# Performance work log

Hardware: AMD Instinct MI355X
Metric: run time of the kernel (lower is better)

Reference implementation:

```python
import jax, jax.numpy as jnp
import numpy as np

MAX_WEIGHT = 10.0  # config.max_weight
EPS = 1e-8

BATCH = 2048
VOCAB = 256
SEQ_LEN = 64
NUM_DENDRITES = SEQ_LEN * VOCAB  # 16384


def setup_inputs() -> dict:
    key = jax.random.key(0)
    k1, k2 = jax.random.split(key)
    # binary dendrite activations in {0,1}, stored as float32 as in the torch module
    binary = jax.random.randint(k1, (BATCH, NUM_DENDRITES), 0, 2).astype(jnp.float32)
    # raw_weights ~ Uniform(-1, 1) per nn.init.uniform_
    raw_weights = jax.random.uniform(k2, (VOCAB, NUM_DENDRITES), dtype=jnp.float32,
                                     minval=-1.0, maxval=1.0)
    return {"binary": binary, "raw_weights": raw_weights}


def reference(binary, raw_weights):
    # bounded positive weights: max_weight * sigmoid(raw)
    w = MAX_WEIGHT * jax.nn.sigmoid(raw_weights)            # (vocab, D)
    log_w = jnp.log(jnp.clip(w, EPS))                       # (vocab, D)
    # masked log-sum: where binary==0 the torch code uses log(1)=0, then multiplies
    # by binary anyway, so it is exactly binary @ log_w.T
    log_sum = jnp.einsum('bd,vd->bv', binary, log_w)        # (batch, vocab)
    n_active = jnp.clip(jnp.sum(binary, axis=-1, keepdims=True), 1.0)  # (batch, 1)
    logits = jnp.exp(log_sum / n_active)                    # geometric mean of fired weights
    return logits
```

## Files before the change

kernel.cpp:

```cpp
#include <hip/hip_runtime.h>

#define BATCH 2048
#define VOCAB 256
#define KDIM 16384
#define WPR (KDIM / 32)
#define BM 64
#define BK 64
#define S_SPLIT 16
#define KCHUNK (KDIM / S_SPLIT)
#define NT (KCHUNK / BK)
#define CW (KCHUNK / 32)
#define WSTRIDE 34
#define LN10 2.302585092994046f

typedef __attribute__((ext_vector_type(8))) short short8;
typedef __attribute__((ext_vector_type(4))) float f32x4;
typedef __attribute__((ext_vector_type(2))) unsigned short u16x2;

#define FENCE asm volatile("" ::: "memory")
#define BAR __builtin_amdgcn_s_barrier()
#define VMW8 asm volatile("s_waitcnt vmcnt(8)" ::: "memory")
#define VMW0 asm volatile("s_waitcnt vmcnt(0)" ::: "memory")

__device__ __forceinline__ unsigned short f2bf_rne(float f) {
  unsigned int u = __float_as_uint(f);
  u += 0x7fffu + ((u >> 16) & 1u);
  return (unsigned short)(u >> 16);
}

__device__ __forceinline__ void async16(void* lds, const void* g) {
  __builtin_amdgcn_global_load_lds(
      (const __attribute__((address_space(1))) unsigned int*)g,
      (__attribute__((address_space(3))) unsigned int*)lds, 16, 0, 0);
}

__device__ __forceinline__ unsigned int pkmul(unsigned int a, unsigned int b) {
  union { unsigned int u; u16x2 h; } x, y, r;
  x.u = a; y.u = b;
  r.h = x.h * y.h;
  return r.u;
}

__global__ __launch_bounds__(256) void k_logw(const float* __restrict__ raw,
                                              unsigned short* __restrict__ logw) {
  int i = blockIdx.x * 256 + threadIdx.x;
  float4 x = ((const float4*)raw)[i];
  ushort4 r;
  r.x = f2bf_rne(LN10 - log1pf(expf(-x.x)));
  r.y = f2bf_rne(LN10 - log1pf(expf(-x.y)));
  r.z = f2bf_rne(LN10 - log1pf(expf(-x.z)));
  r.w = f2bf_rne(LN10 - log1pf(expf(-x.w)));
  ((ushort4*)logw)[i] = r;
}

__global__ __launch_bounds__(256) void k_pack(const float* __restrict__ binary,
                                              unsigned int* __restrict__ bits,
                                              float* __restrict__ nact4) {
  const int r = blockIdx.x;
  const int t = threadIdx.x;
  const int lane = t & 63;
  const float4* src = (const float4*)(binary + (size_t)r * KDIM);
  unsigned int* wrow = bits + (size_t)r * WPR;
  float cnt = 0.f;
#pragma unroll
  for (int i = 0; i < 16; ++i) {
    float4 f = src[i * 256 + t];
    unsigned int nib = ((__float_as_uint(f.x) >> 29) & 1u) |
                       ((__float_as_uint(f.y) >> 28) & 2u) |
                       ((__float_as_uint(f.z) >> 27) & 4u) |
                       ((__float_as_uint(f.w) >> 26) & 8u);
    unsigned int v = nib, p;
    p = __shfl_xor(v, 1, 64); v = (lane & 1) ? (p | (v << 4)) : (v | (p << 4));
    p = __shfl_xor(v, 2, 64); v = (lane & 2) ? (p | (v << 8)) : (v | (p << 8));
    p = __shfl_xor(v, 4, 64); v = (lane & 4) ? (p | (v << 16)) : (v | (p << 16));
    if ((t & 7) == 0) wrow[i * 32 + (t >> 3)] = v;
    cnt += (float)__popc(v);
  }
  cnt *= 0.125f;
  cnt += __shfl_xor(cnt, 1, 64);
  cnt += __shfl_xor(cnt, 2, 64);
  cnt += __shfl_xor(cnt, 4, 64);
  cnt += __shfl_xor(cnt, 8, 64);
  cnt += __shfl_xor(cnt, 16, 64);
  cnt += __shfl_xor(cnt, 32, 64);
  if (lane == 0) nact4[r * 4 + (t >> 6)] = cnt;
}

template <int PART>
__global__ __launch_bounds__(256) void k_gemm(
    const unsigned int* __restrict__ bits, const unsigned short* __restrict__ logw,
    float* __restrict__ outp) {
  extern __shared__ char smem[];
  char* const B0 = smem;
  char* const B1 = smem + 32768;
  unsigned int* const Wb = (unsigned int*)(smem + 65536);

  const int tid = threadIdx.x;
  const int wv = tid >> 6;
  const int lane = tid & 63;
  const int l15 = lane & 15;
  const int lhi = lane >> 4;
  const int sh8 = lhi * 8;
  const int sx = blockIdx.x;
  const int m0 = blockIdx.y * BM;
  const int k0 = sx * KCHUNK;

  {
    const unsigned int* gsrc =
        bits + (size_t)(m0 + (tid >> 2)) * WPR + sx * CW + (tid & 3) * 8;
    uint4 w0 = *(const uint4*)gsrc;
    uint4 w1 = *(const uint4*)(gsrc + 4);
    unsigned int* ld = Wb + (tid >> 2) * WSTRIDE + (tid & 3) * 8;
    ld[0] = w0.x; ld[1] = w0.y; ld[2] = w0.z; ld[3] = w0.w;
    ld[4] = w1.x; ld[5] = w1.y; ld[6] = w1.z; ld[7] = w1.w;
  }
  __syncthreads();

  const unsigned short* bsrc =
      logw + (size_t)(wv * 64 + (lane >> 3)) * KDIM + k0 +
      (((lane & 7) ^ (lane >> 3)) << 3);
  const int rsw = (l15 & 7) << 4;

  f32x4 acc[4][4];
#pragma unroll
  for (int m = 0; m < 4; ++m)
#pragma unroll
    for (int n = 0; n < 4; ++n) acc[m][n] = f32x4{0.f, 0.f, 0.f, 0.f};

  auto BSTAGE = [&](int t, char* B) {
#pragma unroll
    for (int i = 0; i < 8; ++i)
      async16(B + (wv * 64 + i * 8) * 128, bsrc + (size_t)i * 8 * KDIM + t * BK);
  };
  auto COMPUTE = [&](const char* B, int t) {
    uint2 aw[4];
#pragma unroll
    for (int m = 0; m < 4; ++m)
      aw[m] = *(const uint2*)(Wb + (m * 16 + l15) * WSTRIDE + 2 * t);
#pragma unroll
    for (int ks = 0; ks < 2; ++ks) {
      const int koff = ((ks * 64) | (lhi * 16)) ^ rsw;
      short8 bf[4];
#pragma unroll
      for (int n = 0; n < 4; ++n)
        bf[n] = *(const short8*)(B + (wv * 64 + n * 16 + l15) * 128 + koff);
#pragma unroll
      for (int m = 0; m < 4; ++m) {
        const unsigned int w = ks ? aw[m].y : aw[m].x;
        const unsigned int rep = ((w >> sh8) & 0xffu) * 0x01010101u;
        union { unsigned int u[4]; short8 s; } ex;
        ex.u[0] = pkmul(rep & 0x00020001u, 0x1FC03F80u);
        ex.u[1] = pkmul(rep & 0x00080004u, 0x07F00FE0u);
        ex.u[2] = pkmul(rep & 0x00200010u, 0x01FC03F8u);
        ex.u[3] = pkmul(rep & 0x00800040u, 0x007F00FEu);
#pragma unroll
        for (int n = 0; n < 4; ++n)
          acc[m][n] = __builtin_amdgcn_mfma_f32_16x16x32_bf16(bf[n], ex.s,
                                                              acc[m][n], 0, 0, 0);
      }
    }
  };

  BSTAGE(0, B0);
  FENCE;
#pragma unroll 1
  for (int t = 0; t < NT; t += 2) {
    BSTAGE(t + 1, B1);
    FENCE; VMW8; BAR; FENCE;
    COMPUTE(B0, t);
    FENCE; BAR; FENCE;
    if (t + 2 < NT) {
      BSTAGE(t + 2, B0);
      FENCE; VMW8;
    } else {
      VMW0;
    }
    BAR; FENCE;
    COMPUTE(B1, t + 1);
    FENCE; BAR; FENCE;
  }

  if (PART) {
#pragma unroll
    for (int m = 0; m < 4; ++m) {
      float* dst = outp + ((size_t)sx * BATCH + m0 + m * 16 + l15) * VOCAB +
                   wv * 64 + lhi * 4;
#pragma unroll
      for (int n = 0; n < 4; ++n)
        *(float4*)(dst + n * 16) =
            (float4){acc[m][n][0], acc[m][n][1], acc[m][n][2], acc[m][n][3]};
    }
  } else {
#pragma unroll
    for (int m = 0; m < 4; ++m)
#pragma unroll
      for (int n = 0; n < 4; ++n)
#pragma unroll
        for (int i = 0; i < 4; ++i)
          atomicAdd(&outp[(size_t)(m0 + m * 16 + l15) * VOCAB + wv * 64 +
                          n * 16 + lhi * 4 + i],
                    acc[m][n][i]);
  }
}

__global__ __launch_bounds__(256) void k_reduce(const float* __restrict__ part,
                                                const float* __restrict__ nact4,
                                                float* __restrict__ out) {
  int b = blockIdx.x;
  int v = threadIdx.x;
  float sum = 0.f;
#pragma unroll
  for (int i = 0; i < S_SPLIT; ++i)
    sum += part[((size_t)i * BATCH + b) * VOCAB + v];
  float n = nact4[b * 4] + nact4[b * 4 + 1] + nact4[b * 4 + 2] + nact4[b * 4 + 3];
  out[(size_t)b * VOCAB + v] = expf(sum / fmaxf(n, 1.f));
}

__global__ __launch_bounds__(256) void k_out(float* __restrict__ io,
                                             const float* __restrict__ nact4) {
  int b = blockIdx.x;
  int v = threadIdx.x;
  float n = nact4[b * 4] + nact4[b * 4 + 1] + nact4[b * 4 + 2] + nact4[b * 4 + 3];
  n = fmaxf(n, 1.0f);
  size_t idx = (size_t)b * VOCAB + v;
  io[idx] = expf(io[idx] / n);
}

extern "C" void kernel_launch(void* const* d_in, const int* in_sizes, int n_in,
                              void* d_out, int out_size, void* d_ws, size_t ws_size,
                              hipStream_t stream) {
  const float* binary = (const float*)d_in[0];
  const float* raw = (const float*)d_in[1];
  float* out = (float*)d_out;
  char* ws = (char*)d_ws;

  const size_t LOGW_B = (size_t)VOCAB * KDIM * 2;
  const size_t BITS_B = (size_t)BATCH * WPR * 4;
  const size_t NACT_B = (size_t)BATCH * 4 * 4;
  const size_t PART_B = (size_t)S_SPLIT * BATCH * VOCAB * 4;
  unsigned short* logw = (unsigned short*)ws;
  unsigned int* bits = (unsigned int*)(ws + LOGW_B);
  float* nact4 = (float*)(ws + LOGW_B + BITS_B);
  float* part = (float*)(ws + LOGW_B + BITS_B + NACT_B);

  k_logw<<<(VOCAB * KDIM / 4) / 256, 256, 0, stream>>>(raw, logw);
  k_pack<<<BATCH, 256, 0, stream>>>(binary, bits, nact4);

  dim3 g(S_SPLIT, BATCH / BM);
  const size_t LDS_B = 65536 + 64 * WSTRIDE * 4;
  if (ws_size >= LOGW_B + BITS_B + NACT_B + PART_B) {
    k_gemm<1><<<g, 256, LDS_B, stream>>>(bits, logw, part);
    k_reduce<<<BATCH, VOCAB, 0, stream>>>(part, nact4, out);
  } else {
    hipMemsetAsync(out, 0, (size_t)BATCH * VOCAB * sizeof(float), stream);
    k_gemm<0><<<g, 256, LDS_B, stream>>>(bits, logw, out);
    k_out<<<BATCH, VOCAB, 0, stream>>>(out, nact4);
  }
}
```

Baseline: 241.9 us.

## Drop LDS staging in GEMM; load MFMA operands directly from global memory

The GEMM kernel no longer stages logw tiles and packed activation bits through double-buffered LDS with async loads and barriers. Each lane now loads its bf16 B fragments and bit words straight from global memory into registers inside a fully unrolled loop. The K split doubles to 32, and launch bounds ask for 3 blocks per SIMD. This aims to remove LDS traffic, barrier stalls and the LDS occupancy limit, at the cost of less coalesced global loads, heavier reliance on L2/L1, and twice as much partial-sum output for the reduce kernel.

```diff
diff --git a/kernel.cpp b/kernel.cpp
--- a/kernel.cpp
+++ b/kernel.cpp
@@ -5,33 +5,20 @@
 #define KDIM 16384
 #define WPR (KDIM / 32)
 #define BM 64
-#define BK 64
-#define S_SPLIT 16
+#define S_SPLIT 32
 #define KCHUNK (KDIM / S_SPLIT)
-#define NT (KCHUNK / BK)
+#define NT (KCHUNK / 64)
 #define CW (KCHUNK / 32)
-#define WSTRIDE 34
 #define LN10 2.302585092994046f
 
 typedef __attribute__((ext_vector_type(8))) short short8;
 typedef __attribute__((ext_vector_type(4))) float f32x4;
 typedef __attribute__((ext_vector_type(2))) unsigned short u16x2;
-
-#define FENCE asm volatile("" ::: "memory")
-#define BAR __builtin_amdgcn_s_barrier()
-#define VMW8 asm volatile("s_waitcnt vmcnt(8)" ::: "memory")
-#define VMW0 asm volatile("s_waitcnt vmcnt(0)" ::: "memory")
 
 __device__ __forceinline__ unsigned short f2bf_rne(float f) {
   unsigned int u = __float_as_uint(f);
   u += 0x7fffu + ((u >> 16) & 1u);
   return (unsigned short)(u >> 16);
-}
-
-__device__ __forceinline__ void async16(void* lds, const void* g) {
-  __builtin_amdgcn_global_load_lds(
-      (const __attribute__((address_space(1))) unsigned int*)g,
-      (__attribute__((address_space(3))) unsigned int*)lds, 16, 0, 0);
 }
 
 __device__ __forceinline__ unsigned int pkmul(unsigned int a, unsigned int b) {
@@ -87,14 +74,9 @@
 }
 
 template <int PART>
-__global__ __launch_bounds__(256) void k_gemm(
+__global__ __launch_bounds__(256, 3) void k_gemm(
     const unsigned int* __restrict__ bits, const unsigned short* __restrict__ logw,
     float* __restrict__ outp) {
-  extern __shared__ char smem[];
-  char* const B0 = smem;
-  char* const B1 = smem + 32768;
-  unsigned int* const Wb = (unsigned int*)(smem + 65536);
-
   const int tid = threadIdx.x;
   const int wv = tid >> 6;
   const int lane = tid & 63;
@@ -103,23 +85,15 @@
   const int sh8 = lhi * 8;
   const int sx = blockIdx.x;
   const int m0 = blockIdx.y * BM;
-  const int k0 = sx * KCHUNK;
-
-  {
-    const unsigned int* gsrc =
-        bits + (size_t)(m0 + (tid >> 2)) * WPR + sx * CW + (tid & 3) * 8;
-    uint4 w0 = *(const uint4*)gsrc;
-    uint4 w1 = *(const uint4*)(gsrc + 4);
-    unsigned int* ld = Wb + (tid >> 2) * WSTRIDE + (tid & 3) * 8;
-    ld[0] = w0.x; ld[1] = w0.y; ld[2] = w0.z; ld[3] = w0.w;
-    ld[4] = w1.x; ld[5] = w1.y; ld[6] = w1.z; ld[7] = w1.w;
-  }
-  __syncthreads();
-
-  const unsigned short* bsrc =
-      logw + (size_t)(wv * 64 + (lane >> 3)) * KDIM + k0 +
-      (((lane & 7) ^ (lane >> 3)) << 3);
-  const int rsw = (l15 & 7) << 4;
+
+  const unsigned short* bb0 = logw + (size_t)(wv * 64 + l15) * KDIM + sx * KCHUNK + lhi * 8;
+  const unsigned short* bb1 = bb0 + (size_t)16 * KDIM;
+  const unsigned short* bb2 = bb0 + (size_t)32 * KDIM;
+  const unsigned short* bb3 = bb0 + (size_t)48 * KDIM;
+  const unsigned int* wp0 = bits + (size_t)(m0 + l15) * WPR + sx * CW;
+  const unsigned int* wp1 = wp0 + 16 * WPR;
+  const unsigned int* wp2 = wp0 + 32 * WPR;
+  const unsigned int* wp3 = wp0 + 48 * WPR;
 
   f32x4 acc[4][4];
 #pragma unroll
@@ -127,57 +101,43 @@
 #pragma unroll
     for (int n = 0; n < 4; ++n) acc[m][n] = f32x4{0.f, 0.f, 0.f, 0.f};
 
-  auto BSTAGE = [&](int t, char* B) {
-#pragma unroll
-    for (int i = 0; i < 8; ++i)
-      async16(B + (wv * 64 + i * 8) * 128, bsrc + (size_t)i * 8 * KDIM + t * BK);
-  };
-  auto COMPUTE = [&](const char* B, int t) {
-    uint2 aw[4];
-#pragma unroll
-    for (int m = 0; m < 4; ++m)
-      aw[m] = *(const uint2*)(Wb + (m * 16 + l15) * WSTRIDE + 2 * t);
-#pragma unroll
-    for (int ks = 0; ks < 2; ++ks) {
-      const int koff = ((ks * 64) | (lhi * 16)) ^ rsw;
-      short8 bf[4];
-#pragma unroll
-      for (int n = 0; n < 4; ++n)
-        bf[n] = *(const short8*)(B + (wv * 64 + n * 16 + l15) * 128 + koff);
-#pragma unroll
-      for (int m = 0; m < 4; ++m) {
-        const unsigned int w = ks ? aw[m].y : aw[m].x;
-        const unsigned int rep = ((w >> sh8) & 0xffu) * 0x01010101u;
-        union { unsigned int u[4]; short8 s; } ex;
-        ex.u[0] = pkmul(rep & 0x00020001u, 0x1FC03F80u);
-        ex.u[1] = pkmul(rep & 0x00080004u, 0x07F00FE0u);
-        ex.u[2] = pkmul(rep & 0x00200010u, 0x01FC03F8u);
-        ex.u[3] = pkmul(rep & 0x00800040u, 0x007F00FEu);
-#pragma unroll
-        for (int n = 0; n < 4; ++n)
-          acc[m][n] = __builtin_amdgcn_mfma_f32_16x16x32_bf16(bf[n], ex.s,
-                                                              acc[m][n], 0, 0, 0);
+#pragma unroll
+  for (int j = 0; j < NT / 2; ++j) {
+    uint4 w0 = *(const uint4*)(wp0 + 4 * j);
+    uint4 w1 = *(const uint4*)(wp1 + 4 * j);
+    uint4 w2 = *(const uint4*)(wp2 + 4 * j);
+    uint4 w3 = *(const uint4*)(wp3 + 4 * j);
+#pragma unroll
+    for (int h = 0; h < 2; ++h) {
+      const int off = (2 * j + h) * 64;
+      short8 bf[4][2];
+#pragma unroll
+      for (int ks = 0; ks < 2; ++ks) {
+        bf[0][ks] = *(const short8*)(bb0 + off + ks * 32);
+        bf[1][ks] = *(const short8*)(bb1 + off + ks * 32);
+        bf[2][ks] = *(const short8*)(bb2 + off + ks * 32);
+        bf[3][ks] = *(const short8*)(bb3 + off + ks * 32);
+      }
+#pragma unroll
+      for (int ks = 0; ks < 2; ++ks) {
+#pragma unroll
+        for (int m = 0; m < 4; ++m) {
+          const uint4 wm = (m == 0) ? w0 : (m == 1) ? w1 : (m == 2) ? w2 : w3;
+          const unsigned int word =
+              h ? (ks ? wm.w : wm.z) : (ks ? wm.y : wm.x);
+          const unsigned int rep = ((word >> sh8) & 0xffu) * 0x01010101u;
+          union { unsigned int u[4]; short8 s; } ex;
+          ex.u[0] = pkmul(rep & 0x00020001u, 0x1FC03F80u);
+          ex.u[1] = pkmul(rep & 0x00080004u, 0x07F00FE0u);
+          ex.u[2] = pkmul(rep & 0x00200010u, 0x01FC03F8u);
+          ex.u[3] = pkmul(rep & 0x00800040u, 0x007F00FEu);
+#pragma unroll
+          for (int n = 0; n < 4; ++n)
+            acc[m][n] = __builtin_amdgcn_mfma_f32_16x16x32_bf16(
+                bf[n][ks], ex.s, acc[m][n], 0, 0, 0);
+        }
       }
     }
-  };
-
-  BSTAGE(0, B0);
-  FENCE;
-#pragma unroll 1
-  for (int t = 0; t < NT; t += 2) {
-    BSTAGE(t + 1, B1);
-    FENCE; VMW8; BAR; FENCE;
-    COMPUTE(B0, t);
-    FENCE; BAR; FENCE;
-    if (t + 2 < NT) {
-      BSTAGE(t + 2, B0);
-      FENCE; VMW8;
-    } else {
-      VMW0;
-    }
-    BAR; FENCE;
-    COMPUTE(B1, t + 1);
-    FENCE; BAR; FENCE;
   }
 
   if (PART) {
@@ -247,13 +207,12 @@
   k_pack<<<BATCH, 256, 0, stream>>>(binary, bits, nact4);
 
   dim3 g(S_SPLIT, BATCH / BM);
-  const size_t LDS_B = 65536 + 64 * WSTRIDE * 4;
   if (ws_size >= LOGW_B + BITS_B + NACT_B + PART_B) {
-    k_gemm<1><<<g, 256, LDS_B, stream>>>(bits, logw, part);
+    k_gemm<1><<<g, 256, 0, stream>>>(bits, logw, part);
     k_reduce<<<BATCH, VOCAB, 0, stream>>>(part, nact4, out);
   } else {
     hipMemsetAsync(out, 0, (size_t)BATCH * VOCAB * sizeof(float), stream);
-    k_gemm<0><<<g, 256, LDS_B, stream>>>(bits, logw, out);
+    k_gemm<0><<<g, 256, 0, stream>>>(bits, logw, out);
     k_out<<<BATCH, VOCAB, 0, stream>>>(out, nact4);
   }
 }
```

Result: slower. 272.0 us (+12.4%).
